# Kernel optimization log

Hardware: AMD Instinct MI355X
Metric: run time of the kernel (lower is better)

Reference implementation:

```python
import jax, jax.numpy as jnp
import numpy as np

HID, INTER, STATE, H, P, K, Q = 1024, 2048, 128, 32, 64, 4, 256
CONV_DIM = INTER + 2 * STATE           # 2304
D_IN = 2 * INTER + 2 * STATE + H       # 4384


def silu(x):
    return x * jax.nn.sigmoid(x)


def setup_inputs() -> dict:
    key = jax.random.key(0)
    ks = jax.random.split(key, 8)
    B, L = 2, 2048
    return {
        "hidden_states": jax.random.normal(ks[0], (B, L, HID), jnp.float32),
        "in_proj_w": jax.random.normal(ks[1], (D_IN, HID), jnp.float32) * 0.02,
        "conv_w": jax.random.normal(ks[2], (CONV_DIM, K), jnp.float32) * 0.2,
        "conv_b": jnp.zeros((CONV_DIM,), jnp.float32),
        "dt_bias": jax.random.normal(ks[3], (H,), jnp.float32) * 0.1,
        "A_log": jnp.log(jax.random.uniform(ks[4], (H,), jnp.float32, 1.0, 16.0)),
        "D": jnp.ones((H,), jnp.float32),
        "norm_weight": jnp.ones((INTER,), jnp.float32),
        "out_proj_w": jax.random.normal(ks[5], (HID, INTER), jnp.float32) * 0.02,
    }


def reference(hidden_states, in_proj_w, conv_w, conv_b, dt_bias, A_log, D,
              norm_weight, out_proj_w):
    b, l, _ = hidden_states.shape
    # in_proj -> [z | xBC | dt_raw]  (d_mlp = 0)
    zxbcdt = hidden_states @ in_proj_w.T                      # [b,l,4384]
    z = zxbcdt[..., :INTER]                                   # [b,l,INTER]
    xBC = zxbcdt[..., INTER:INTER + CONV_DIM]                 # [b,l,CONV_DIM]
    dt_raw = zxbcdt[..., INTER + CONV_DIM:]                   # [b,l,H]

    # causal depthwise conv1d + silu (pad k-1 on the left)
    xp = jnp.pad(xBC.transpose(0, 2, 1), ((0, 0), (0, 0), (K - 1, 0)))
    xc = jax.lax.conv_general_dilated(
        xp, conv_w[:, None, :], (1,), 'VALID',
        feature_group_count=CONV_DIM,
        dimension_numbers=('NCH', 'OIH', 'NCH'))
    xBC = silu(xc + conv_b[None, :, None]).transpose(0, 2, 1)  # [b,l,CONV_DIM]

    x = xBC[..., :INTER]                                       # [b,l,INTER]
    Bm = xBC[..., INTER:INTER + STATE]                         # [b,l,N]
    Cm = xBC[..., INTER + STATE:]                              # [b,l,N]

    dt = jax.nn.softplus(dt_raw + dt_bias)                     # [b,l,H]
    A = -jnp.exp(A_log)                                        # [H]

    # chunked SSD scan (Mamba2), chunk size Q
    nc = l // Q
    xh = x.reshape(b, nc, Q, H, P)
    dtc = dt.reshape(b, nc, Q, H)
    Bc = Bm.reshape(b, nc, Q, STATE)
    Cc = Cm.reshape(b, nc, Q, STATE)

    seg = jnp.cumsum(dtc * A, axis=2)                          # [b,c,Q,H]
    xdt = xh * dtc[..., None]                                  # [b,c,Q,H,P]

    # intra-chunk (diagonal block): causal attention-like form
    CB = jnp.einsum('bcin,bcjn->bcij', Cc, Bc)                 # [b,c,Q,Q]
    diff = seg[:, :, :, None, :] - seg[:, :, None, :, :]       # [b,c,i,j,H]
    mask = jnp.tril(jnp.ones((Q, Q), bool))[None, None, :, :, None]
    Lm = jnp.exp(jnp.where(mask, diff, -1e30))
    M = CB[..., None] * Lm                                     # [b,c,i,j,H]
    Yd = jnp.einsum('bcijh,bcjhp->bcihp', M, xdt)

    # chunk-final states and inter-chunk recurrence
    decay_states = jnp.exp(seg[:, :, -1:, :] - seg)            # [b,c,Q,H]
    states = jnp.einsum('bcjn,bcjhp->bchpn', Bc,
                        xdt * decay_states[..., None])         # [b,c,H,P,N]
    chunk_decay = jnp.exp(seg[:, :, -1, :])                    # [b,c,H]

    def step(carry, inp):
        st, dec = inp
        new = carry * dec[:, :, None, None] + st
        return new, carry  # emit state BEFORE this chunk

    init = jnp.zeros((b, H, P, STATE), dtype=xh.dtype)
    _, prev = jax.lax.scan(step, init,
                           (states.transpose(1, 0, 2, 3, 4),
                            chunk_decay.transpose(1, 0, 2)))
    prev = prev.transpose(1, 0, 2, 3, 4)                       # [b,c,H,P,N]

    Yo = jnp.einsum('bcin,bchpn,bcih->bcihp', Cc, prev, jnp.exp(seg))

    y = (Yd + Yo + D[None, None, None, :, None] * xh).reshape(b, l, INTER)

    # gated RMSNorm (norm_before_gate=False): normalize(y * silu(z)) * w
    yg = y * silu(z)
    yn = yg * jax.lax.rsqrt(jnp.mean(yg * yg, axis=-1, keepdims=True) + 1e-6)
    yn = yn * norm_weight

    return yn @ out_proj_w.T                                   # [b,l,HID]
```

## Files before the change

### kernel.cpp

```cpp
#include <hip/hip_runtime.h>

#define HID      1024
#define INTER    2048
#define STATE    128
#define NH       32
#define PDIM     64
#define KCONV    4
#define QCH      256
#define CONV_DIM (INTER + 2*STATE)
#define DPROJ    (2*INTER + 2*STATE + NH)
#define DPROJ_PAD 4480
#define BATCH    2
#define SEQ      2048
#define NCHUNK   (SEQ / QCH)
#define BL       (BATCH * SEQ)

typedef unsigned short u16;
typedef unsigned int   u32;
typedef u16 u16x8 __attribute__((ext_vector_type(8)));
typedef u16 u16x4 __attribute__((ext_vector_type(4)));
typedef float f32x4 __attribute__((ext_vector_type(4)));
typedef __bf16 bf16x8 __attribute__((ext_vector_type(8)));

static __device__ __forceinline__ u16 f2bf(float f) {
    u32 u = __float_as_uint(f);
    return (u16)((u + 0x7FFFu + ((u >> 16) & 1u)) >> 16);
}
static __device__ __forceinline__ float bf2f(u16 v) {
    return __uint_as_float(((u32)v) << 16);
}
static __device__ __forceinline__ void gload_lds16(const void* g, void* l) {
    __builtin_amdgcn_global_load_lds(
        (const __attribute__((address_space(1))) void*)g,
        (__attribute__((address_space(3))) void*)l, 16, 0, 0);
}
static __device__ __forceinline__ int swz64(int row, int slot) {
    return ((row * 64 + slot * 16) ^ (((row >> 1) & 3) << 4)) >> 1;
}
static __device__ __forceinline__ int swz128(int row, int slot) {
    return ((row * 128 + slot * 16) ^ ((row & 7) << 4)) >> 1;
}

__global__ __launch_bounds__(256)
void cvt_all(const float* __restrict__ hidden, const float* __restrict__ w1,
             const float* __restrict__ w2, u16* __restrict__ Abf,
             u16* __restrict__ Wbf, u16* __restrict__ W2bf) {
    const long nA  = (long)BL * HID;
    const long nW  = (long)DPROJ_PAD * HID;
    const long nWr = (long)DPROJ * HID;
    const long nW2 = (long)HID * INTER;
    long i = ((long)blockIdx.x * 256 + threadIdx.x) * 8;
    const float* src; u16* dst; long j;
    if (i < nA)            { src = hidden; dst = Abf;  j = i; }
    else if (i < nA + nW)  { j = i - nA;
        if (j >= nWr) { *(u16x8*)&Wbf[j] = (u16x8)0; return; }
        src = w1; dst = Wbf; }
    else                   { j = i - nA - nW;
        if (j >= nW2) return;
        src = w2; dst = W2bf; }
    float4 a = *(const float4*)&src[j];
    float4 b = *(const float4*)&src[j + 4];
    u16x8 o;
    o[0] = f2bf(a.x); o[1] = f2bf(a.y); o[2] = f2bf(a.z); o[3] = f2bf(a.w);
    o[4] = f2bf(b.x); o[5] = f2bf(b.y); o[6] = f2bf(b.z); o[7] = f2bf(b.w);
    *(u16x8*)&dst[j] = o;
}

__global__ __launch_bounds__(256)
void gemm_in_kernel(const u16* __restrict__ A, const u16* __restrict__ W,
                    u16* __restrict__ Cb, float* __restrict__ dtside,
                    int Nstride, int Nreal, int K) {
    __shared__ __attribute__((aligned(16))) u16 As[128 * 64];
    __shared__ __attribute__((aligned(16))) u16 Ws[128 * 64];
    const int gx = gridDim.x;
    const int nwg = gx * gridDim.y;
    const int wg = blockIdx.y * gx + blockIdx.x;
    const int nid = (wg & 7) * (nwg >> 3) + (wg >> 3);
    const int bm = (nid / gx) * 128;
    const int bn = (nid % gx) * 128;

    const int t = threadIdx.x;
    const int lane = t & 63;
    const int wave = t >> 6;
    const int wr = wave >> 1, wc = wave & 1;
    const int fr = lane & 15;
    const int fq = lane >> 4;
    const int fr7 = fr & 7;

    f32x4 acc[4][4];
#pragma unroll
    for (int m = 0; m < 4; ++m)
#pragma unroll
        for (int n = 0; n < 4; ++n) acc[m][n] = 0;

    const u16* Ag = A + (size_t)bm * K;
    const u16* Wg = W + (size_t)bn * K;

    for (int kt = 0; kt < K; kt += 64) {
#pragma unroll
        for (int q = 0; q < 4; ++q) {
            int ch = t + 256 * q;
            int row = ch >> 3, slot = ch & 7;
            int ksrc = kt + (slot ^ (row & 7)) * 8;
            gload_lds16(Ag + (size_t)row * K + ksrc, &As[ch * 8]);
            gload_lds16(Wg + (size_t)row * K + ksrc, &Ws[ch * 8]);
        }
        __syncthreads();
#pragma unroll
        for (int ks = 0; ks < 2; ++ks) {
            bf16x8 af[4], bw[4];
#pragma unroll
            for (int mi = 0; mi < 4; ++mi) {
                int r = wr * 64 + mi * 16 + fr;
                af[mi] = *(const bf16x8*)&As[r * 64 + ((ks * 4 + fq) ^ fr7) * 8];
            }
#pragma unroll
            for (int ni = 0; ni < 4; ++ni) {
                int r = wc * 64 + ni * 16 + fr;
                bw[ni] = *(const bf16x8*)&Ws[r * 64 + ((ks * 4 + fq) ^ fr7) * 8];
            }
#pragma unroll
            for (int mi = 0; mi < 4; ++mi)
#pragma unroll
                for (int ni = 0; ni < 4; ++ni)
                    acc[mi][ni] = __builtin_amdgcn_mfma_f32_16x16x32_bf16(
                        af[mi], bw[ni], acc[mi][ni], 0, 0, 0);
        }
        __syncthreads();
    }

#pragma unroll
    for (int m = 0; m < 4; ++m)
#pragma unroll
        for (int n = 0; n < 4; ++n) {
            int col = bn + wc * 64 + n * 16 + fr;
            if (col >= Nreal) continue;
            int row0 = bm + wr * 64 + m * 16 + fq * 4;
#pragma unroll
            for (int r = 0; r < 4; ++r)
                Cb[(size_t)(row0 + r) * Nstride + col] = f2bf(acc[m][n][r]);
        }
    if (bn + 128 > INTER + CONV_DIM) {
#pragma unroll
        for (int m = 0; m < 4; ++m)
#pragma unroll
            for (int n = 0; n < 4; ++n) {
                int col = bn + wc * 64 + n * 16 + fr;
                if (col < INTER + CONV_DIM || col >= Nreal) continue;
                int row0 = bm + wr * 64 + m * 16 + fq * 4;
#pragma unroll
                for (int r = 0; r < 4; ++r)
                    dtside[(size_t)(row0 + r) * NH +
                           (col - INTER - CONV_DIM)] = acc[m][n][r];
            }
    }
}

__global__ __launch_bounds__(256)
void gemm_ks_kernel(const u16* __restrict__ A, const u16* __restrict__ W,
                    float* __restrict__ Cp, int M, int N, int Kfull, int Ksub) {
    __shared__ __attribute__((aligned(16))) u16 As[128 * 64];
    __shared__ __attribute__((aligned(16))) u16 Ws[128 * 64];
    const int gx = gridDim.x;
    const int nwg = gx * gridDim.y;
    const int wg = blockIdx.y * gx + blockIdx.x;
    const int nid = (wg & 7) * (nwg >> 3) + (wg >> 3);
    const int bm = (nid / gx) * 128;
    const int bn = (nid % gx) * 128;
    const int k0 = blockIdx.z * Ksub;

    const int t = threadIdx.x;
    const int lane = t & 63;
    const int wave = t >> 6;
    const int wr = wave >> 1, wc = wave & 1;
    const int fr = lane & 15;
    const int fq = lane >> 4;
    const int fr7 = fr & 7;

    f32x4 acc[4][4];
#pragma unroll
    for (int m = 0; m < 4; ++m)
#pragma unroll
        for (int n = 0; n < 4; ++n) acc[m][n] = 0;

    const u16* Ag = A + (size_t)bm * Kfull + k0;
    const u16* Wg = W + (size_t)bn * Kfull + k0;

    for (int kt = 0; kt < Ksub; kt += 64) {
#pragma unroll
        for (int q = 0; q < 4; ++q) {
            int ch = t + 256 * q;
            int row = ch >> 3, slot = ch & 7;
            int ksrc = kt + (slot ^ (row & 7)) * 8;
            gload_lds16(Ag + (size_t)row * Kfull + ksrc, &As[ch * 8]);
            gload_lds16(Wg + (size_t)row * Kfull + ksrc, &Ws[ch * 8]);
        }
        __syncthreads();
#pragma unroll
        for (int ks = 0; ks < 2; ++ks) {
            bf16x8 af[4], bw[4];
#pragma unroll
            for (int mi = 0; mi < 4; ++mi) {
                int r = wr * 64 + mi * 16 + fr;
                af[mi] = *(const bf16x8*)&As[r * 64 + ((ks * 4 + fq) ^ fr7) * 8];
            }
#pragma unroll
            for (int ni = 0; ni < 4; ++ni) {
                int r = wc * 64 + ni * 16 + fr;
                bw[ni] = *(const bf16x8*)&Ws[r * 64 + ((ks * 4 + fq) ^ fr7) * 8];
            }
#pragma unroll
            for (int mi = 0; mi < 4; ++mi)
#pragma unroll
                for (int ni = 0; ni < 4; ++ni)
                    acc[mi][ni] = __builtin_amdgcn_mfma_f32_16x16x32_bf16(
                        af[mi], bw[ni], acc[mi][ni], 0, 0, 0);
        }
        __syncthreads();
    }

    float* Cz = Cp + (size_t)blockIdx.z * M * N;
#pragma unroll
    for (int m = 0; m < 4; ++m)
#pragma unroll
        for (int n = 0; n < 4; ++n) {
            int col = bn + wc * 64 + n * 16 + fr;
            int row0 = bm + wr * 64 + m * 16 + fq * 4;
#pragma unroll
            for (int r = 0; r < 4; ++r)
                Cz[(size_t)(row0 + r) * N + col] = acc[m][n][r];
        }
}

__global__ __launch_bounds__(256)
void addred_kernel(const float* __restrict__ p, float* __restrict__ o, long n) {
    long i = ((long)blockIdx.x * 256 + threadIdx.x) * 4;
    if (i >= n) return;
    float4 a = *(const float4*)&p[i];
    float4 b = *(const float4*)&p[n + i];
    float4 r = make_float4(a.x + b.x, a.y + b.y, a.z + b.z, a.w + b.w);
    *(float4*)&o[i] = r;
}

__global__ __launch_bounds__(256)
void convT_kernel(const u16* __restrict__ zxb,
                  const float* __restrict__ conv_w,
                  const float* __restrict__ conv_b,
                  u16* __restrict__ xT, u16* __restrict__ BT,
                  u16* __restrict__ Bbf, u16* __restrict__ Cbf) {
    __shared__ float s[64][65];
    const int c0 = blockIdx.x * 64;
    const int l0 = blockIdx.y * 64;
    const int b  = blockIdx.z;
    const int t  = threadIdx.x;
    const int j  = t & 63;
    const int g  = t >> 6;
    const int cg = c0 + j;
    const float w0 = conv_w[cg * 4 + 0], w1 = conv_w[cg * 4 + 1];
    const float w2 = conv_w[cg * 4 + 2], w3 = conv_w[cg * 4 + 3];
    const float bias = conv_b[cg];
    const u16* col = zxb + (size_t)b * SEQ * DPROJ + INTER + cg;
    int lbase = l0 + g * 16;
    float h3, h2, h1;
    h3 = (lbase - 3 >= 0) ? bf2f(col[(size_t)(lbase - 3) * DPROJ]) : 0.f;
    h2 = (lbase - 2 >= 0) ? bf2f(col[(size_t)(lbase - 2) * DPROJ]) : 0.f;
    h1 = (lbase - 1 >= 0) ? bf2f(col[(size_t)(lbase - 1) * DPROJ]) : 0.f;
#pragma unroll
    for (int k = 0; k < 16; ++k) {
        int l = lbase + k;
        float x0 = bf2f(col[(size_t)l * DPROJ]);
        float v = bias + h3 * w0 + h2 * w1 + h1 * w2 + x0 * w3;
        v = v / (1.f + __expf(-v));
        h3 = h2; h2 = h1; h1 = x0;
        s[g * 16 + k][j] = v;
        if (cg >= INTER) {
            int n = cg - INTER;
            if (n < STATE)
                Bbf[(size_t)(b * SEQ + l) * STATE + n] = f2bf(v);
            else
                Cbf[(size_t)(b * SEQ + l) * STATE + (n - STATE)] = f2bf(v);
        }
    }
    if (c0 >= INTER + STATE) return;
    __syncthreads();
    const int rr = t >> 2;
    const int lch = (t & 3) * 16;
    int cgout = c0 + rr;
    u16* orow;
    if (cgout < INTER) orow = xT + (size_t)(b * SEQ + cgout) * SEQ;
    else               orow = BT + (size_t)(b * STATE + (cgout - INTER)) * SEQ;
    u16x8 o0, o1;
#pragma unroll
    for (int e = 0; e < 8; ++e) o0[e] = f2bf(s[lch + e][rr]);
#pragma unroll
    for (int e = 0; e < 8; ++e) o1[e] = f2bf(s[lch + 8 + e][rr]);
    *(u16x8*)&orow[l0 + lch]     = o0;
    *(u16x8*)&orow[l0 + lch + 8] = o1;
}

__global__ __launch_bounds__(256)
void dtseg_kernel(const float* __restrict__ dtraw,
                  const float* __restrict__ dt_bias,
                  const float* __restrict__ A_log,
                  float* __restrict__ dt_out,
                  float* __restrict__ seg_out) {
    int bid = blockIdx.x;
    int h = bid & 31, c = (bid >> 5) & 7, b = bid >> 8;
    int i = threadIdx.x;
    int bl = b * SEQ + c * QCH + i;
    float x = dtraw[(size_t)bl * NH + h] + dt_bias[h];
    float dtv = (x > 20.f) ? x : log1pf(expf(x));
    dt_out[bl * NH + h] = dtv;
    float Ah = -expf(A_log[h]);
    __shared__ float s[QCH];
    s[i] = dtv * Ah;
    __syncthreads();
    for (int off = 1; off < QCH; off <<= 1) {
        float add = (i >= off) ? s[i - off] : 0.f;
        __syncthreads();
        s[i] += add;
        __syncthreads();
    }
    seg_out[bl * NH + h] = s[i];
}

__global__ __launch_bounds__(256)
void cb_kernel(const u16* __restrict__ Cbf, const u16* __restrict__ Bbf,
               float* __restrict__ CB) {
    const int jt = blockIdx.x, it = blockIdx.y;
    if (jt > it) return;
    const int bc = blockIdx.z;
    const int b = bc >> 3, c = bc & 7;
    __shared__ __attribute__((aligned(16))) u16 Ct[64 * 32];
    __shared__ __attribute__((aligned(16))) u16 Bt[64 * 32];
    const int t = threadIdx.x;
    const int lane = t & 63, wave = t >> 6;
    const int wr = wave >> 1, wc = wave & 1;
    const int fr = lane & 15, fq = lane >> 4;
    const int l0 = b * SEQ + c * QCH;
    f32x4 acc[2][2];
#pragma unroll
    for (int m = 0; m < 2; ++m)
#pragma unroll
        for (int n = 0; n < 2; ++n) acc[m][n] = 0;
    const int srow = t >> 2, sslot = t & 3;
    for (int n0 = 0; n0 < STATE; n0 += 32) {
        gload_lds16(Cbf + (size_t)(l0 + it * 64 + srow) * STATE + n0 +
                        8 * (sslot ^ ((srow >> 1) & 3)), &Ct[t * 8]);
        gload_lds16(Bbf + (size_t)(l0 + jt * 64 + srow) * STATE + n0 +
                        8 * (sslot ^ ((srow >> 1) & 3)), &Bt[t * 8]);
        __syncthreads();
        bf16x8 af[2], bw[2];
#pragma unroll
        for (int m = 0; m < 2; ++m)
            af[m] = *(const bf16x8*)&Ct[swz64(wr * 32 + m * 16 + fr, fq)];
#pragma unroll
        for (int n = 0; n < 2; ++n)
            bw[n] = *(const bf16x8*)&Bt[swz64(wc * 32 + n * 16 + fr, fq)];
#pragma unroll
        for (int m = 0; m < 2; ++m)
#pragma unroll
            for (int n = 0; n < 2; ++n)
                acc[m][n] = __builtin_amdgcn_mfma_f32_16x16x32_bf16(
                    af[m], bw[n], acc[m][n], 0, 0, 0);
        __syncthreads();
    }
#pragma unroll
    for (int m = 0; m < 2; ++m)
#pragma unroll
        for (int n = 0; n < 2; ++n) {
            int i = it * 64 + wr * 32 + m * 16 + fq * 4;
            int jj = jt * 64 + wc * 32 + n * 16 + fr;
#pragma unroll
            for (int r = 0; r < 4; ++r)
                CB[((size_t)bc * QCH + i + r) * QCH + jj] = acc[m][n][r];
        }
}

__global__ __launch_bounds__(256)
void states_kernel(const u16* __restrict__ xT, const u16* __restrict__ BT,
                   const float* __restrict__ dt, const float* __restrict__ seg,
                   u16* __restrict__ statesb) {
    int bid = blockIdx.x;
    int h = bid & 31, c = (bid >> 5) & 7, b = bid >> 8;
    __shared__ float dd[QCH];
    __shared__ __attribute__((aligned(16))) u16 At[64 * 32];
    __shared__ __attribute__((aligned(16))) u16 Bt[128 * 32];
    const int t = threadIdx.x;
    const int lane = t & 63, wave = t >> 6;
    const int wr = wave >> 1, wc = wave & 1;
    const int fr = lane & 15, fq = lane >> 4;
    const int l0 = b * SEQ + c * QCH;
    {
        float seg_last = seg[(size_t)(l0 + QCH - 1) * NH + h];
        dd[t] = dt[(size_t)(l0 + t) * NH + h] *
                __expf(seg_last - seg[(size_t)(l0 + t) * NH + h]);
    }
    __syncthreads();
    f32x4 acc[2][4];
#pragma unroll
    for (int m = 0; m < 2; ++m)
#pragma unroll
        for (int n = 0; n < 4; ++n) acc[m][n] = 0;
    const int ap = t >> 2, ajs = t & 3;
    const u16* xrow = xT + (size_t)(b * SEQ + h * PDIM + ap) * SEQ + c * QCH;
    for (int j0 = 0; j0 < QCH; j0 += 32) {
        u16x8 v = *(const u16x8*)&xrow[j0 + ajs * 8];
        u16x8 o;
#pragma unroll
        for (int e = 0; e < 8; ++e)
            o[e] = f2bf(bf2f(v[e]) * dd[j0 + ajs * 8 + e]);
        *(u16x8*)&At[swz64(ap, ajs)] = o;
#pragma unroll
        for (int q = 0; q < 2; ++q) {
            int chunk = t + 256 * q;
            int row = chunk >> 2, slot = chunk & 3;
            gload_lds16(BT + (size_t)(b * STATE + row) * SEQ + c * QCH + j0 +
                            8 * (slot ^ ((row >> 1) & 3)), &Bt[chunk * 8]);
        }
        __syncthreads();
        bf16x8 af[2], bw[4];
#pragma unroll
        for (int m = 0; m < 2; ++m)
            af[m] = *(const bf16x8*)&At[swz64(wr * 32 + m * 16 + fr, fq)];
#pragma unroll
        for (int n = 0; n < 4; ++n)
            bw[n] = *(const bf16x8*)&Bt[swz64(wc * 64 + n * 16 + fr, fq)];
#pragma unroll
        for (int m = 0; m < 2; ++m)
#pragma unroll
            for (int n = 0; n < 4; ++n)
                acc[m][n] = __builtin_amdgcn_mfma_f32_16x16x32_bf16(
                    af[m], bw[n], acc[m][n], 0, 0, 0);
        __syncthreads();
    }
    size_t base = ((((size_t)b * NCHUNK + c) * NH + h) * PDIM) * STATE;
#pragma unroll
    for (int m = 0; m < 2; ++m)
#pragma unroll
        for (int n = 0; n < 4; ++n) {
            int p = wr * 32 + m * 16 + fq * 4;
            int nn = wc * 64 + n * 16 + fr;
#pragma unroll
            for (int r = 0; r < 4; ++r)
                statesb[base + (size_t)(p + r) * STATE + nn] = f2bf(acc[m][n][r]);
        }
}

__global__ void scan_kernel(const u16* __restrict__ statesb,
                            const float* __restrict__ seg,
                            u16* __restrict__ prevbf) {
    int tid = blockIdx.x * blockDim.x + threadIdx.x;
    int n = tid & 127, p = (tid >> 7) & 63, h = (tid >> 13) & 31, b = tid >> 18;
    float carry = 0.f;
    for (int c = 0; c < NCHUNK; ++c) {
        size_t idx = ((((size_t)b * NCHUNK + c) * NH + h) * PDIM + p) * STATE + n;
        float st = bf2f(statesb[idx]);
        prevbf[idx] = f2bf(carry);
        float dec = __expf(seg[(size_t)(b*SEQ + c*QCH + QCH - 1) * NH + h]);
        carry = carry * dec + st;
    }
}

__global__ __launch_bounds__(256)
void ydo_kernel(const u16* __restrict__ xT, const u16* __restrict__ Cbf,
                const u16* __restrict__ prevbf, const float* __restrict__ CB,
                const float* __restrict__ dt, const float* __restrict__ seg,
                const float* __restrict__ Dv, u16* __restrict__ yb) {
    int bid = blockIdx.x;
    int h = bid & 31, c = (bid >> 5) & 7, b = bid >> 8;
    __shared__ float seg_s[QCH], sge_s[QCH], dtv_s[QCH];
    __shared__ __attribute__((aligned(16))) u16 big[QCH * 64];
    __shared__ __attribute__((aligned(16))) u16 small[64 * 64];
    const int t = threadIdx.x;
    const int lane = t & 63, w = t >> 6;
    const int fr = lane & 15, fq = lane >> 4;
    const int l0 = b * SEQ + c * QCH;
    {
        float sv = seg[(size_t)(l0 + t) * NH + h];
        seg_s[t] = sv;
        sge_s[t] = __expf(sv);
        dtv_s[t] = dt[(size_t)(l0 + t) * NH + h];
    }
    __syncthreads();
    f32x4 acc[4][4];
#pragma unroll
    for (int m = 0; m < 4; ++m)
#pragma unroll
        for (int n = 0; n < 4; ++n) acc[m][n] = 0;

    const size_t pvbase = ((((size_t)b * NCHUNK + c) * NH + h) * PDIM) * STATE;
    for (int ks = 0; ks < 4; ++ks) {
#pragma unroll
        for (int q = 0; q < 4; ++q) {
            int chunk = t + 256 * q;
            int row = chunk >> 2, slot = chunk & 3;
            gload_lds16(Cbf + (size_t)(l0 + row) * STATE + ks * 32 +
                            8 * (slot ^ ((row >> 1) & 3)), &big[chunk * 8]);
        }
        {
            int row = t >> 2, slot = t & 3;
            gload_lds16(prevbf + pvbase + (size_t)row * STATE + ks * 32 +
                            8 * (slot ^ ((row >> 1) & 3)), &small[t * 8]);
        }
        __syncthreads();
        bf16x8 af[4], bw[4];
#pragma unroll
        for (int m = 0; m < 4; ++m)
            af[m] = *(const bf16x8*)&big[swz64(64 * m + 16 * w + fr, fq)];
#pragma unroll
        for (int n = 0; n < 4; ++n)
            bw[n] = *(const bf16x8*)&small[swz64(16 * n + fr, fq)];
#pragma unroll
        for (int m = 0; m < 4; ++m)
#pragma unroll
            for (int n = 0; n < 4; ++n)
                acc[m][n] = __builtin_amdgcn_mfma_f32_16x16x32_bf16(
                    af[m], bw[n], acc[m][n], 0, 0, 0);
        __syncthreads();
    }
#pragma unroll
    for (int m = 0; m < 4; ++m)
#pragma unroll
        for (int n = 0; n < 4; ++n)
#pragma unroll
            for (int r = 0; r < 4; ++r)
                acc[m][n][r] *= sge_s[64 * m + 16 * w + fq * 4 + r];

    const float* CBrow = CB + (size_t)(b * NCHUNK + c) * QCH * QCH;
    for (int jt = 0; jt < 4; ++jt) {
        const int j0 = jt * 64;
        const int mcol = t & 63;
        for (int r = j0 + (t >> 6); r < QCH; r += 4) {
            float v = 0.f;
            if (mcol <= r - j0)
                v = CBrow[(size_t)r * QCH + j0 + mcol] *
                    __expf(seg_s[r] - seg_s[j0 + mcol]) * dtv_s[j0 + mcol];
            big[((r * 128 + mcol * 2) ^ ((r & 7) << 4)) >> 1] = f2bf(v);
        }
#pragma unroll
        for (int q = 0; q < 2; ++q) {
            int chunk = t + 256 * q;
            int row = chunk >> 3, slot = chunk & 7;
            gload_lds16(xT + (size_t)(b * SEQ + h * PDIM + row) * SEQ +
                            c * QCH + j0 + 8 * (slot ^ (row & 7)),
                        &small[chunk * 8]);
        }
        __syncthreads();
#pragma unroll
        for (int ks = 0; ks < 2; ++ks) {
#pragma unroll
            for (int m = 0; m < 4; ++m) {
                if (64 * m + 16 * w >= j0) {
                    bf16x8 af = *(const bf16x8*)
                        &big[swz128(64 * m + 16 * w + fr, ks * 4 + fq)];
#pragma unroll
                    for (int n = 0; n < 4; ++n) {
                        bf16x8 bw = *(const bf16x8*)
                            &small[swz128(16 * n + fr, ks * 4 + fq)];
                        acc[m][n] = __builtin_amdgcn_mfma_f32_16x16x32_bf16(
                            af, bw, acc[m][n], 0, 0, 0);
                    }
                }
            }
        }
        __syncthreads();
    }
    const float Dh = Dv[h];
#pragma unroll
    for (int m = 0; m < 4; ++m) {
        int i = 64 * m + 16 * w + fq * 4;
#pragma unroll
        for (int n = 0; n < 4; ++n) {
            int p = 16 * n + fr;
            u16x4 xv = *(const u16x4*)&xT[(size_t)(b * SEQ + h * PDIM + p) * SEQ +
                                          c * QCH + i];
#pragma unroll
            for (int r = 0; r < 4; ++r)
                yb[(size_t)(l0 + i + r) * INTER + h * PDIM + p] =
                    f2bf(acc[m][n][r] + Dh * bf2f(xv[r]));
        }
    }
}

__global__ __launch_bounds__(256)
void gatenorm_kernel(u16* __restrict__ yb, const u16* __restrict__ zxb,
                     const float* __restrict__ nw) {
    int bl = blockIdx.x;
    int t = threadIdx.x;
    u16x8 yv8 = *(const u16x8*)&yb[(size_t)bl * INTER + t * 8];
    u16x8 zv8 = *(const u16x8*)&zxb[(size_t)bl * DPROJ + t * 8];
    float g[8];
    float ss = 0.f;
#pragma unroll
    for (int i = 0; i < 8; ++i) {
        float yv = bf2f(yv8[i]), zv = bf2f(zv8[i]);
        g[i] = yv * (zv / (1.f + expf(-zv)));
        ss += g[i] * g[i];
    }
    for (int off = 32; off > 0; off >>= 1) ss += __shfl_xor(ss, off, 64);
    __shared__ float red[4];
    if ((t & 63) == 0) red[t >> 6] = ss;
    __syncthreads();
    float tot = red[0] + red[1] + red[2] + red[3];
    float scale = rsqrtf(tot / INTER + 1e-6f);
    const float* nwp = nw + t * 8;
    u16x8 o;
#pragma unroll
    for (int i = 0; i < 8; ++i) o[i] = f2bf(g[i] * scale * nwp[i]);
    *(u16x8*)&yb[(size_t)bl * INTER + t * 8] = o;
}

extern "C" void kernel_launch(void* const* d_in, const int* in_sizes, int n_in,
                              void* d_out, int out_size, void* d_ws, size_t ws_size,
                              hipStream_t stream) {
    const float* hidden     = (const float*)d_in[0];
    const float* in_proj_w  = (const float*)d_in[1];
    const float* conv_w     = (const float*)d_in[2];
    const float* conv_b     = (const float*)d_in[3];
    const float* dt_bias    = (const float*)d_in[4];
    const float* A_log      = (const float*)d_in[5];
    const float* Dv         = (const float*)d_in[6];
    const float* norm_w     = (const float*)d_in[7];
    const float* out_proj_w = (const float*)d_in[8];
    float* out = (float*)d_out;

    u16* wsu    = (u16*)d_ws;
    u16* zxb    = wsu;
    u16* statesb= zxb    + (size_t)BL * DPROJ;
    u16* prevbf = statesb+ (size_t)BATCH*NCHUNK*NH*PDIM*STATE;
    u16* yb     = prevbf + (size_t)BATCH*NCHUNK*NH*PDIM*STATE;
    u16* xT     = yb     + (size_t)BL * INTER;
    u16* BT     = xT     + (size_t)BL * INTER;
    u16* Bbf    = BT     + (size_t)BATCH * STATE * SEQ;
    u16* Cbf    = Bbf    + (size_t)BL * STATE;
    u16* W2bf   = Cbf    + (size_t)BL * STATE;
    float* dtraw = (float*)(W2bf + (size_t)HID * INTER);
    float* dtb   = dtraw + (size_t)BL * NH;
    float* segb  = dtb   + (size_t)BL * NH;
    float* CB    = segb  + (size_t)BL * NH;
    u16* Abf = statesb;
    u16* Wbf = statesb + (size_t)BL * HID;
    float* kpart = (float*)zxb;

    {
        long total = (long)BL*HID + (long)DPROJ_PAD*HID + (long)HID*INTER;
        cvt_all<<<(int)(total / 2048), 256, 0, stream>>>(
            hidden, in_proj_w, out_proj_w, Abf, Wbf, W2bf);
    }

    gemm_in_kernel<<<dim3(DPROJ_PAD/128, BL/128), 256, 0, stream>>>(
        Abf, Wbf, zxb, dtraw, DPROJ, DPROJ, HID);

    dtseg_kernel<<<BATCH * NCHUNK * NH, 256, 0, stream>>>(
        dtraw, dt_bias, A_log, dtb, segb);
    convT_kernel<<<dim3(CONV_DIM/64, SEQ/64, BATCH), 256, 0, stream>>>(
        zxb, conv_w, conv_b, xT, BT, Bbf, Cbf);
    cb_kernel<<<dim3(4, 4, BATCH*NCHUNK), 256, 0, stream>>>(Cbf, Bbf, CB);
    states_kernel<<<BATCH * NCHUNK * NH, 256, 0, stream>>>(
        xT, BT, dtb, segb, statesb);
    scan_kernel<<<(BATCH * NH * PDIM * STATE) / 256, 256, 0, stream>>>(
        statesb, segb, prevbf);
    ydo_kernel<<<BATCH * NCHUNK * NH, 256, 0, stream>>>(
        xT, Cbf, prevbf, CB, dtb, segb, Dv, yb);
    gatenorm_kernel<<<BL, 256, 0, stream>>>(yb, zxb, norm_w);

    gemm_ks_kernel<<<dim3(HID/128, BL/128, 2), 256, 0, stream>>>(
        yb, W2bf, kpart, BL, HID, INTER, INTER/2);
    addred_kernel<<<((long)BL*HID)/1024, 256, 0, stream>>>(
        kpart, out, (long)BL*HID);
}
```

Measured before the change: 228.0 us.

## Store CB in bf16, widen ydo K-tiles, vectorize CB masking loop

cb_kernel now writes the C·B^T matrix as bf16 instead of fp32. ydo_kernel reads it back with 4-wide vector loads, which halves the CB traffic that every head re-reads. The inter-chunk GEMM in ydo_kernel now loads 64-wide K tiles with a 128-byte swizzle, so the K loop needs two barrier rounds instead of four. gatenorm switches to the fast __expf. Rounding CB to bf16 before the decay scaling adds some precision loss.

After: 196.8 us. 1.16x faster.

```diff
diff --git a/kernel.cpp b/kernel.cpp
--- a/kernel.cpp
+++ b/kernel.cpp
@@ -326,7 +326,7 @@
 
 __global__ __launch_bounds__(256)
 void cb_kernel(const u16* __restrict__ Cbf, const u16* __restrict__ Bbf,
-               float* __restrict__ CB) {
+               u16* __restrict__ CBbf) {
     const int jt = blockIdx.x, it = blockIdx.y;
     if (jt > it) return;
     const int bc = blockIdx.z;
@@ -373,7 +373,7 @@
             int jj = jt * 64 + wc * 32 + n * 16 + fr;
 #pragma unroll
             for (int r = 0; r < 4; ++r)
-                CB[((size_t)bc * QCH + i + r) * QCH + jj] = acc[m][n][r];
+                CBbf[((size_t)bc * QCH + i + r) * QCH + jj] = f2bf(acc[m][n][r]);
         }
 }
 
@@ -464,7 +464,7 @@
 
 __global__ __launch_bounds__(256)
 void ydo_kernel(const u16* __restrict__ xT, const u16* __restrict__ Cbf,
-                const u16* __restrict__ prevbf, const float* __restrict__ CB,
+                const u16* __restrict__ prevbf, const u16* __restrict__ CBbf,
                 const float* __restrict__ dt, const float* __restrict__ seg,
                 const float* __restrict__ Dv, u16* __restrict__ yb) {
     int bid = blockIdx.x;
@@ -490,33 +490,40 @@
         for (int n = 0; n < 4; ++n) acc[m][n] = 0;
 
     const size_t pvbase = ((((size_t)b * NCHUNK + c) * NH + h) * PDIM) * STATE;
-    for (int ks = 0; ks < 4; ++ks) {
-#pragma unroll
-        for (int q = 0; q < 4; ++q) {
-            int chunk = t + 256 * q;
-            int row = chunk >> 2, slot = chunk & 3;
-            gload_lds16(Cbf + (size_t)(l0 + row) * STATE + ks * 32 +
-                            8 * (slot ^ ((row >> 1) & 3)), &big[chunk * 8]);
-        }
-        {
-            int row = t >> 2, slot = t & 3;
-            gload_lds16(prevbf + pvbase + (size_t)row * STATE + ks * 32 +
-                            8 * (slot ^ ((row >> 1) & 3)), &small[t * 8]);
-        }
-        __syncthreads();
-        bf16x8 af[4], bw[4];
-#pragma unroll
-        for (int m = 0; m < 4; ++m)
-            af[m] = *(const bf16x8*)&big[swz64(64 * m + 16 * w + fr, fq)];
-#pragma unroll
-        for (int n = 0; n < 4; ++n)
-            bw[n] = *(const bf16x8*)&small[swz64(16 * n + fr, fq)];
-#pragma unroll
-        for (int m = 0; m < 4; ++m)
+    for (int kc = 0; kc < 2; ++kc) {
+#pragma unroll
+        for (int q = 0; q < 8; ++q) {
+            int ch = t + 256 * q;
+            int row = ch >> 3, slot = ch & 7;
+            gload_lds16(Cbf + (size_t)(l0 + row) * STATE + kc * 64 +
+                            8 * (slot ^ (row & 7)), &big[ch * 8]);
+        }
+#pragma unroll
+        for (int q = 0; q < 2; ++q) {
+            int ch = t + 256 * q;
+            int row = ch >> 3, slot = ch & 7;
+            gload_lds16(prevbf + pvbase + (size_t)row * STATE + kc * 64 +
+                            8 * (slot ^ (row & 7)), &small[ch * 8]);
+        }
+        __syncthreads();
+#pragma unroll
+        for (int ks2 = 0; ks2 < 2; ++ks2) {
+            bf16x8 af[4], bw[4];
+#pragma unroll
+            for (int m = 0; m < 4; ++m)
+                af[m] = *(const bf16x8*)&big[swz128(64 * m + 16 * w + fr,
+                                                   ks2 * 4 + fq)];
 #pragma unroll
             for (int n = 0; n < 4; ++n)
-                acc[m][n] = __builtin_amdgcn_mfma_f32_16x16x32_bf16(
-                    af[m], bw[n], acc[m][n], 0, 0, 0);
+                bw[n] = *(const bf16x8*)&small[swz128(16 * n + fr,
+                                                      ks2 * 4 + fq)];
+#pragma unroll
+            for (int m = 0; m < 4; ++m)
+#pragma unroll
+                for (int n = 0; n < 4; ++n)
+                    acc[m][n] = __builtin_amdgcn_mfma_f32_16x16x32_bf16(
+                        af[m], bw[n], acc[m][n], 0, 0, 0);
+        }
         __syncthreads();
     }
 #pragma unroll
@@ -527,16 +534,23 @@
             for (int r = 0; r < 4; ++r)
                 acc[m][n][r] *= sge_s[64 * m + 16 * w + fq * 4 + r];
 
-    const float* CBrow = CB + (size_t)(b * NCHUNK + c) * QCH * QCH;
+    const u16* CBrow = CBbf + (size_t)(b * NCHUNK + c) * QCH * QCH;
     for (int jt = 0; jt < 4; ++jt) {
         const int j0 = jt * 64;
-        const int mcol = t & 63;
-        for (int r = j0 + (t >> 6); r < QCH; r += 4) {
-            float v = 0.f;
-            if (mcol <= r - j0)
-                v = CBrow[(size_t)r * QCH + j0 + mcol] *
-                    __expf(seg_s[r] - seg_s[j0 + mcol]) * dtv_s[j0 + mcol];
-            big[((r * 128 + mcol * 2) ^ ((r & 7) << 4)) >> 1] = f2bf(v);
+        const int c4 = (t & 15) * 4;
+        for (int r = j0 + (t >> 4); r < QCH; r += 16) {
+            u16x4 cb4 = *(const u16x4*)&CBrow[(size_t)r * QCH + j0 + c4];
+            u16x4 o4;
+#pragma unroll
+            for (int e = 0; e < 4; ++e) {
+                int mcol = c4 + e;
+                float v = 0.f;
+                if (mcol <= r - j0)
+                    v = bf2f(cb4[e]) * __expf(seg_s[r] - seg_s[j0 + mcol]) *
+                        dtv_s[j0 + mcol];
+                o4[e] = f2bf(v);
+            }
+            *(u16x4*)&big[((r * 128 + c4 * 2) ^ ((r & 7) << 4)) >> 1] = o4;
         }
 #pragma unroll
         for (int q = 0; q < 2; ++q) {
@@ -595,7 +609,7 @@
 #pragma unroll
     for (int i = 0; i < 8; ++i) {
         float yv = bf2f(yv8[i]), zv = bf2f(zv8[i]);
-        g[i] = yv * (zv / (1.f + expf(-zv)));
+        g[i] = yv * (zv / (1.f + __expf(-zv)));
         ss += g[i] * g[i];
     }
     for (int off = 32; off > 0; off >>= 1) ss += __shfl_xor(ss, off, 64);
@@ -638,7 +652,7 @@
     float* dtraw = (float*)(W2bf + (size_t)HID * INTER);
     float* dtb   = dtraw + (size_t)BL * NH;
     float* segb  = dtb   + (size_t)BL * NH;
-    float* CB    = segb  + (size_t)BL * NH;
+    u16*  CBbf   = (u16*)(segb + (size_t)BL * NH);
     u16* Abf = statesb;
     u16* Wbf = statesb + (size_t)BL * HID;
     float* kpart = (float*)zxb;
@@ -656,13 +670,13 @@
         dtraw, dt_bias, A_log, dtb, segb);
     convT_kernel<<<dim3(CONV_DIM/64, SEQ/64, BATCH), 256, 0, stream>>>(
         zxb, conv_w, conv_b, xT, BT, Bbf, Cbf);
-    cb_kernel<<<dim3(4, 4, BATCH*NCHUNK), 256, 0, stream>>>(Cbf, Bbf, CB);
+    cb_kernel<<<dim3(4, 4, BATCH*NCHUNK), 256, 0, stream>>>(Cbf, Bbf, CBbf);
     states_kernel<<<BATCH * NCHUNK * NH, 256, 0, stream>>>(
         xT, BT, dtb, segb, statesb);
     scan_kernel<<<(BATCH * NH * PDIM * STATE) / 256, 256, 0, stream>>>(
         statesb, segb, prevbf);
     ydo_kernel<<<BATCH * NCHUNK * NH, 256, 0, stream>>>(
-        xT, Cbf, prevbf, CB, dtb, segb, Dv, yb);
+        xT, Cbf, prevbf, CBbf, dtb, segb, Dv, yb);
     gatenorm_kernel<<<BL, 256, 0, stream>>>(yb, zxb, norm_w);
 
     gemm_ks_kernel<<<dim3(HID/128, BL/128, 2), 256, 0, stream>>>(
```
